# Optimization experiments

Hardware: AMD Instinct MI355X
Metric: run time of the kernel (lower is better)

Reference implementation:

```python
import jax, jax.numpy as jnp
import numpy as np

N_NODES = 50000
N_EDGES = 800000
IN_DIM = 128
HID = 256
BN_EPS = 1e-5
NEG_SLOPE = 0.01


def setup_inputs() -> dict:
    key = jax.random.key(0)
    ks = jax.random.split(key, 8)
    inp = {
        "x": jax.random.normal(ks[0], (N_NODES, IN_DIM), dtype=jnp.float32),
        "src": jax.random.randint(ks[1], (N_EDGES,), 0, N_NODES, dtype=jnp.int32),
        "dst": jax.random.randint(ks[2], (N_EDGES,), 0, N_NODES, dtype=jnp.int32),
        # layer 0 MLP (in->hid->hid) + BN params
        "w1_0": jax.random.normal(ks[3], (IN_DIM, HID), dtype=jnp.float32) / np.sqrt(IN_DIM),
        "b1_0": jnp.zeros((HID,), jnp.float32),
        "w2_0": jax.random.normal(ks[4], (HID, HID), dtype=jnp.float32) / np.sqrt(HID),
        "b2_0": jnp.zeros((HID,), jnp.float32),
        "g0": jnp.ones((HID,), jnp.float32),
        "be0": jnp.zeros((HID,), jnp.float32),
        "m0": jnp.zeros((HID,), jnp.float32),
        "v0": jnp.ones((HID,), jnp.float32),
        # layers 1..2 stacked (hid->hid->hid) + BN params
        "w1_r": jax.random.normal(ks[5], (2, HID, HID), dtype=jnp.float32) / np.sqrt(HID),
        "b1_r": jnp.zeros((2, HID), jnp.float32),
        "w2_r": jax.random.normal(ks[6], (2, HID, HID), dtype=jnp.float32) / np.sqrt(HID),
        "b2_r": jnp.zeros((2, HID), jnp.float32),
        "g_r": jnp.ones((2, HID), jnp.float32),
        "be_r": jnp.zeros((2, HID), jnp.float32),
        "m_r": jnp.zeros((2, HID), jnp.float32),
        "v_r": jnp.ones((2, HID), jnp.float32),
    }
    return inp


def _gin_layer(h, src, dst, w1, b1, w2, b2, g, be, m, v, last):
    # GINConv (eps=0): (1+eps)*h + sum_{j in N(i)} h_j  via gather + scatter-add
    agg = jax.ops.segment_sum(h[src], dst, num_segments=N_NODES)
    z = h + agg
    # 2-layer MLP (dropout is identity in eval)
    z = jax.nn.leaky_relu(z @ w1 + b1, NEG_SLOPE)
    z = z @ w2 + b2
    # BatchNorm1d (eval: running stats)
    z = (z - m) * jax.lax.rsqrt(v + BN_EPS) * g + be
    if not last:
        z = jax.nn.leaky_relu(z, NEG_SLOPE)
    return z


def reference(x, src, dst, w1_0, b1_0, w2_0, b2_0, g0, be0, m0, v0,
              w1_r, b1_r, w2_r, b2_r, g_r, be_r, m_r, v_r):
    h = _gin_layer(x, src, dst, w1_0, b1_0, w2_0, b2_0, g0, be0, m0, v0, last=False)
    for l in range(2):
        h = _gin_layer(h, src, dst, w1_r[l], b1_r[l], w2_r[l], b2_r[l],
                       g_r[l], be_r[l], m_r[l], v_r[l], last=(l == 1))
    return h
```

## Files before the change

kernel.cpp:

```cpp
#include <hip/hip_runtime.h>
#include <hip/hip_bf16.h>
#include <stdint.h>

#define NN 50000
#define NE 800000
#define IND 128
#define HID 256
#define MPAD 50048
#define NBLK 49

#define NCH 64
#define CHSZ 12500
#define NRG 8
#define RGSZ 6250

typedef unsigned int uint32;
typedef unsigned short ushort_t;
typedef __attribute__((ext_vector_type(8))) short short8;
typedef __attribute__((ext_vector_type(4))) float f32x4;

typedef const __attribute__((address_space(1))) void* gptr_t;
typedef __attribute__((address_space(3))) void* lptr_t;

__device__ __forceinline__ ushort_t f2b(float f) {
  uint32 u = __float_as_uint(f);
  u = (u + 0x7fffu + ((u >> 16) & 1u)) >> 16;
  return (ushort_t)u;
}
__device__ __forceinline__ float blo(uint32 u) { return __uint_as_float(u << 16); }
__device__ __forceinline__ float bhi(uint32 u) { return __uint_as_float(u & 0xffff0000u); }
__device__ __forceinline__ uint32 pack2(float a, float b) {
  return (uint32)f2b(a) | ((uint32)f2b(b) << 16);
}

__global__ __launch_bounds__(256) void histp_k(const int* __restrict__ dst,
                                               uint32* __restrict__ partial,
                                               int* __restrict__ rnk) {
  __shared__ uint32 lh[RGSZ];
  const int c = blockIdx.x & (NCH - 1);
  const int rg = blockIdx.x >> 6;
  const int r0 = rg * RGSZ;
  for (int i = threadIdx.x; i < RGSZ; i += 256) lh[i] = 0;
  __syncthreads();
  const int e0 = c * CHSZ;
  for (int i = threadIdx.x; i < CHSZ; i += 256) {
    int e = e0 + i;
    int d = dst[e] - r0;
    if ((unsigned)d < (unsigned)RGSZ) rnk[e] = (int)atomicAdd(&lh[d], 1u);
  }
  __syncthreads();
  uint32* po = partial + (size_t)c * NN + r0;
  for (int i = threadIdx.x; i < RGSZ; i += 256) po[i] = lh[i];
}

__global__ void coff_k(uint32* __restrict__ partial, int* __restrict__ cnt) {
  int bin = blockIdx.x * 256 + threadIdx.x;
  if (bin >= NN) return;
  uint32 run = 0;
#pragma unroll
  for (int c = 0; c < NCH; c++) {
    uint32 t = partial[(size_t)c * NN + bin];
    partial[(size_t)c * NN + bin] = run;
    run += t;
  }
  cnt[bin] = (int)run;
}

__global__ void bsum_k(const int* __restrict__ cnt, int* __restrict__ bsum) {
  __shared__ int ws[16];
  const int tid = threadIdx.x, ln = tid & 63, wv = tid >> 6;
  int i = blockIdx.x * 1024 + tid;
  int v = (i < NN) ? cnt[i] : 0;
#pragma unroll
  for (int d = 32; d; d >>= 1) v += __shfl_down(v, d, 64);
  if (ln == 0) ws[wv] = v;
  __syncthreads();
  if (tid < 16) {
    int s = ws[tid];
#pragma unroll
    for (int d = 8; d; d >>= 1) s += __shfl_down(s, d, 64);
    if (tid == 0) bsum[blockIdx.x] = s;
  }
}

__global__ void bscan_k(int* __restrict__ bsum, int* __restrict__ rp) {
  int tid = threadIdx.x;
  int v = (tid < NBLK) ? bsum[tid] : 0;
  int x = v;
#pragma unroll
  for (int d = 1; d < 64; d <<= 1) {
    int t = __shfl_up(x, d, 64);
    if (tid >= d) x += t;
  }
  if (tid < NBLK) bsum[tid] = x - v;
  if (tid == 0) rp[NN] = NE;
}

__global__ void scan2_k(const int* __restrict__ cnt, const int* __restrict__ bsum,
                        int* __restrict__ rp) {
  __shared__ int ws[16];
  const int tid = threadIdx.x, ln = tid & 63, wv = tid >> 6;
  int i = blockIdx.x * 1024 + tid;
  int v = (i < NN) ? cnt[i] : 0;
  int x = v;
#pragma unroll
  for (int d = 1; d < 64; d <<= 1) {
    int t = __shfl_up(x, d, 64);
    if (ln >= d) x += t;
  }
  if (ln == 63) ws[wv] = x;
  __syncthreads();
  if (tid < 16) {
    int s = ws[tid];
#pragma unroll
    for (int d = 1; d < 16; d <<= 1) {
      int t = __shfl_up(s, d, 64);
      if (tid >= d) s += t;
    }
    ws[tid] = s;
  }
  __syncthreads();
  int excl = x - v + (wv ? ws[wv - 1] : 0) + bsum[blockIdx.x];
  if (i < NN) rp[i] = excl;
}

__global__ void scat2_k(const int* __restrict__ src, const int* __restrict__ dst,
                        const int* __restrict__ rp, const uint32* __restrict__ partial,
                        const int* __restrict__ rnk, int* __restrict__ esrc) {
  int e = blockIdx.x * 256 + threadIdx.x;
  if (e < NE) {
    int d = dst[e];
    int c = e / CHSZ;
    int pos = rp[d] + (int)partial[(size_t)c * NN + d] + rnk[e];
    esrc[pos] = src[e];
  }
}

__global__ void prep_k(const float* __restrict__ w1_0, const float* __restrict__ w2_0,
                       const float* __restrict__ w1_r, const float* __restrict__ w2_r,
                       const float* b1_0, const float* b2_0, const float* g0,
                       const float* be0, const float* m0, const float* v0,
                       const float* b1_r, const float* b2_r, const float* g_r,
                       const float* be_r, const float* m_r, const float* v_r,
                       ushort_t* __restrict__ wt,
                       float* bi1, float* sc2, float* bi2) {
  const int which = blockIdx.y;
  if (which < 6) {
    const int n = blockIdx.x, k = threadIdx.x;
    const float* w; ushort_t* o; int K = HID;
    switch (which) {
      case 0: w = w1_0; o = wt; K = IND; break;
      case 1: w = w2_0; o = wt + HID * IND; break;
      case 2: w = w1_r; o = wt + HID * IND + 1 * HID * HID; break;
      case 3: w = w2_r; o = wt + HID * IND + 2 * HID * HID; break;
      case 4: w = w1_r + HID * HID; o = wt + HID * IND + 3 * HID * HID; break;
      default: w = w2_r + HID * HID; o = wt + HID * IND + 4 * HID * HID; break;
    }
    if (k < K) o[n * K + k] = f2b(w[(size_t)k * HID + n]);
  } else {
    const int l = blockIdx.x;
    if (l >= 3) return;
    const int j = threadIdx.x;
    float b1, b2, g, be, m, v;
    if (l == 0) { b1 = b1_0[j]; b2 = b2_0[j]; g = g0[j]; be = be0[j]; m = m0[j]; v = v0[j]; }
    else { int o = (l - 1) * HID + j; b1 = b1_r[o]; b2 = b2_r[o]; g = g_r[o]; be = be_r[o]; m = m_r[o]; v = v_r[o]; }
    int o = l * HID + j;
    bi1[o] = b1;
    float s = g * rsqrtf(v + 1e-5f);
    sc2[o] = s;
    bi2[o] = (b2 - m) * s + be;
  }
}

__global__ void x2b_k(const float* __restrict__ x, ushort_t* __restrict__ xb) {
  int i = blockIdx.x * 256 + threadIdx.x;
  const int n = NN * IND / 2;
  if (i < n) {
    float2 f = ((const float2*)x)[i];
    ((uint32*)xb)[i] = pack2(f.x, f.y);
  }
}

__global__ void agg256_k(const ushort_t* __restrict__ h, const int* __restrict__ rp,
                         const int* __restrict__ esrc, ushort_t* __restrict__ z) {
  int wid = threadIdx.x >> 6, lane = threadIdx.x & 63;
  int node = blockIdx.x * 4 + wid;
  if (node >= NN) return;
  const uint2* hp = (const uint2*)h;
  uint2 v = hp[(size_t)node * 64 + lane];
  float a0 = blo(v.x), a1 = bhi(v.x), a2 = blo(v.y), a3 = bhi(v.y);
  int e0 = rp[node], e1 = rp[node + 1];
  int e = e0;
  for (; e + 8 <= e1; e += 8) {
    int s[8];
#pragma unroll
    for (int q = 0; q < 8; q++) s[q] = esrc[e + q];
    uint2 u[8];
#pragma unroll
    for (int q = 0; q < 8; q++) u[q] = hp[(size_t)s[q] * 64 + lane];
#pragma unroll
    for (int q = 0; q < 8; q++) {
      a0 += blo(u[q].x); a1 += bhi(u[q].x); a2 += blo(u[q].y); a3 += bhi(u[q].y);
    }
  }
  for (; e < e1; e++) {
    int s = esrc[e];
    uint2 u = hp[(size_t)s * 64 + lane];
    a0 += blo(u.x); a1 += bhi(u.x); a2 += blo(u.y); a3 += bhi(u.y);
  }
  uint2 o; o.x = pack2(a0, a1); o.y = pack2(a2, a3);
  ((uint2*)z)[(size_t)node * 64 + lane] = o;
}

__global__ void agg128_k(const ushort_t* __restrict__ h, const int* __restrict__ rp,
                         const int* __restrict__ esrc, ushort_t* __restrict__ z) {
  int wid = threadIdx.x >> 6, lane = threadIdx.x & 63;
  int node = blockIdx.x * 4 + wid;
  if (node >= NN) return;
  const uint32* hp = (const uint32*)h;
  uint32 v = hp[(size_t)node * 64 + lane];
  float a0 = blo(v), a1 = bhi(v);
  int e0 = rp[node], e1 = rp[node + 1];
  int e = e0;
  for (; e + 8 <= e1; e += 8) {
    int s[8];
#pragma unroll
    for (int q = 0; q < 8; q++) s[q] = esrc[e + q];
    uint32 u[8];
#pragma unroll
    for (int q = 0; q < 8; q++) u[q] = hp[(size_t)s[q] * 64 + lane];
#pragma unroll
    for (int q = 0; q < 8; q++) { a0 += blo(u[q]); a1 += bhi(u[q]); }
  }
  for (; e < e1; e++) {
    int s = esrc[e];
    uint32 u = hp[(size_t)s * 64 + lane];
    a0 += blo(u); a1 += bhi(u);
  }
  ((uint32*)z)[(size_t)node * 64 + lane] = pack2(a0, a1);
}

__global__ __launch_bounds__(256, 2) void fgemm_k(
    const ushort_t* __restrict__ A, const ushort_t* __restrict__ B1t,
    const ushort_t* __restrict__ B2t, const float* __restrict__ bi1,
    const float* __restrict__ sc2, const float* __restrict__ bi2,
    void* __restrict__ out, int K1, int lrelu2, int f32out) {
  __shared__ ushort_t As[64 * 32];
  __shared__ ushort_t Bs[256 * 32];
  __shared__ ushort_t C1s[64 * 264];
  const int tid = threadIdx.x;
  const int lane = tid & 63;
  const int wid = tid >> 6;
  const int m0 = blockIdx.x * 64;
  const int srow = tid >> 2;
  const int sch = (tid & 3) * 8;
  const int fr = lane & 15;
  const int fk = (lane >> 4) * 8;
  const int er = lane >> 4;
  const int ec = lane & 15;

  f32x4 zero = {0.f, 0.f, 0.f, 0.f};
  f32x4 acc[4][4];
#pragma unroll
  for (int i = 0; i < 4; i++)
#pragma unroll
    for (int j = 0; j < 4; j++) acc[i][j] = zero;

  for (int kk = 0; kk < K1; kk += 32) {
    __builtin_amdgcn_global_load_lds((gptr_t)(A + (size_t)(m0 + srow) * K1 + kk + sch),
                                     (lptr_t)(As + srow * 32 + sch), 16, 0, 0);
#pragma unroll
    for (int p = 0; p < 4; p++)
      __builtin_amdgcn_global_load_lds(
          (gptr_t)(B1t + (size_t)(p * 64 + srow) * K1 + kk + sch),
          (lptr_t)(Bs + (p * 64 + srow) * 32 + sch), 16, 0, 0);
    __syncthreads();
    short8 af[4], bfv[4];
#pragma unroll
    for (int i = 0; i < 4; i++)
      af[i] = *(const short8*)(As + (i * 16 + fr) * 32 + fk);
#pragma unroll
    for (int j = 0; j < 4; j++)
      bfv[j] = *(const short8*)(Bs + (wid * 64 + j * 16 + fr) * 32 + fk);
#pragma unroll
    for (int i = 0; i < 4; i++)
#pragma unroll
      for (int j = 0; j < 4; j++)
        acc[i][j] = __builtin_amdgcn_mfma_f32_16x16x32_bf16(af[i], bfv[j], acc[i][j], 0, 0, 0);
    __syncthreads();
  }

#pragma unroll
  for (int j = 0; j < 4; j++) {
    int col = wid * 64 + j * 16 + ec;
    float b = bi1[col];
#pragma unroll
    for (int i = 0; i < 4; i++) {
#pragma unroll
      for (int r = 0; r < 4; r++) {
        int row = i * 16 + er * 4 + r;
        float v = acc[i][j][r] + b;
        v = (v > 0.f) ? v : 0.01f * v;
        C1s[row * 264 + col] = f2b(v);
      }
    }
  }
  __syncthreads();

  f32x4 acc2[4][4];
#pragma unroll
  for (int i = 0; i < 4; i++)
#pragma unroll
    for (int j = 0; j < 4; j++) acc2[i][j] = zero;

  for (int kk = 0; kk < HID; kk += 32) {
#pragma unroll
    for (int p = 0; p < 4; p++)
      __builtin_amdgcn_global_load_lds(
          (gptr_t)(B2t + (size_t)(p * 64 + srow) * HID + kk + sch),
          (lptr_t)(Bs + (p * 64 + srow) * 32 + sch), 16, 0, 0);
    __syncthreads();
    short8 af[4], bfv[4];
#pragma unroll
    for (int i = 0; i < 4; i++)
      af[i] = *(const short8*)(C1s + (i * 16 + fr) * 264 + kk + fk);
#pragma unroll
    for (int j = 0; j < 4; j++)
      bfv[j] = *(const short8*)(Bs + (wid * 64 + j * 16 + fr) * 32 + fk);
#pragma unroll
    for (int i = 0; i < 4; i++)
#pragma unroll
      for (int j = 0; j < 4; j++)
        acc2[i][j] = __builtin_amdgcn_mfma_f32_16x16x32_bf16(af[i], bfv[j], acc2[i][j], 0, 0, 0);
    __syncthreads();
  }

#pragma unroll
  for (int j = 0; j < 4; j++) {
    int col = wid * 64 + j * 16 + ec;
    float s = sc2[col], b = bi2[col];
#pragma unroll
    for (int i = 0; i < 4; i++) {
#pragma unroll
      for (int r = 0; r < 4; r++) {
        int row = m0 + i * 16 + er * 4 + r;
        float v = acc2[i][j][r] * s + b;
        if (lrelu2) v = (v > 0.f) ? v : 0.01f * v;
        if (row < NN) {
          if (f32out) ((float*)out)[(size_t)row * HID + col] = v;
          else        ((ushort_t*)out)[(size_t)row * HID + col] = f2b(v);
        }
      }
    }
  }
}

extern "C" void kernel_launch(void* const* d_in, const int* in_sizes, int n_in,
                              void* d_out, int out_size, void* d_ws, size_t ws_size,
                              hipStream_t stream) {
  const float* x    = (const float*)d_in[0];
  const int*   src  = (const int*)d_in[1];
  const int*   dst  = (const int*)d_in[2];
  const float* w1_0 = (const float*)d_in[3];
  const float* b1_0 = (const float*)d_in[4];
  const float* w2_0 = (const float*)d_in[5];
  const float* b2_0 = (const float*)d_in[6];
  const float* g0   = (const float*)d_in[7];
  const float* be0  = (const float*)d_in[8];
  const float* m0   = (const float*)d_in[9];
  const float* v0   = (const float*)d_in[10];
  const float* w1_r = (const float*)d_in[11];
  const float* b1_r = (const float*)d_in[12];
  const float* w2_r = (const float*)d_in[13];
  const float* b2_r = (const float*)d_in[14];
  const float* g_r  = (const float*)d_in[15];
  const float* be_r = (const float*)d_in[16];
  const float* m_r  = (const float*)d_in[17];
  const float* v_r  = (const float*)d_in[18];

  char* ws = (char*)d_ws;
  size_t off = 0;
  auto alloc = [&](size_t bytes) {
    void* p = ws + off;
    off = (off + bytes + 255) & ~(size_t)255;
    return p;
  };
  ushort_t* bufA  = (ushort_t*)alloc((size_t)MPAD * HID * 2);
  ushort_t* bufB  = (ushort_t*)alloc((size_t)MPAD * HID * 2);
  ushort_t* xb    = (ushort_t*)alloc((size_t)MPAD * IND * 2);
  int*      rp    = (int*)alloc((NN + 1) * sizeof(int));
  int*      cnt   = (int*)alloc(NN * sizeof(int));
  int*      bsum  = (int*)alloc(NBLK * sizeof(int));
  int*      esrc  = (int*)alloc((size_t)NE * sizeof(int));
  ushort_t* wt    = (ushort_t*)alloc(((size_t)HID * IND + 5 * (size_t)HID * HID) * 2);
  float*    bi1   = (float*)alloc(3 * HID * sizeof(float));
  float*    sc2   = (float*)alloc(3 * HID * sizeof(float));
  float*    bi2   = (float*)alloc(3 * HID * sizeof(float));
  (void)ws_size; (void)in_sizes; (void)n_in; (void)out_size;

  uint32* partial = (uint32*)bufA;
  int*    rnk     = (int*)bufB;

  ushort_t* w1_0t = wt;
  ushort_t* w2_0t = wt + HID * IND;
  ushort_t* w1r0t = wt + HID * IND + 1 * HID * HID;
  ushort_t* w2r0t = wt + HID * IND + 2 * HID * HID;
  ushort_t* w1r1t = wt + HID * IND + 3 * HID * HID;
  ushort_t* w2r1t = wt + HID * IND + 4 * HID * HID;

  histp_k<<<NCH * NRG, 256, 0, stream>>>(dst, partial, rnk);
  coff_k<<<(NN + 255) / 256, 256, 0, stream>>>(partial, cnt);
  bsum_k<<<NBLK, 1024, 0, stream>>>(cnt, bsum);
  bscan_k<<<1, 64, 0, stream>>>(bsum, rp);
  scan2_k<<<NBLK, 1024, 0, stream>>>(cnt, bsum, rp);
  scat2_k<<<(NE + 255) / 256, 256, 0, stream>>>(src, dst, rp, partial, rnk, esrc);

  prep_k<<<dim3(HID, 7), 256, 0, stream>>>(w1_0, w2_0, w1_r, w2_r,
                                           b1_0, b2_0, g0, be0, m0, v0,
                                           b1_r, b2_r, g_r, be_r, m_r, v_r,
                                           wt, bi1, sc2, bi2);
  x2b_k<<<(NN * IND / 2 + 255) / 256, 256, 0, stream>>>(x, xb);

  const int GG = MPAD / 64;
  agg128_k<<<NN / 4, 256, 0, stream>>>(xb, rp, esrc, bufA);
  fgemm_k<<<GG, 256, 0, stream>>>(bufA, w1_0t, w2_0t, bi1, sc2, bi2, bufB, IND, 1, 0);
  agg256_k<<<NN / 4, 256, 0, stream>>>(bufB, rp, esrc, bufA);
  fgemm_k<<<GG, 256, 0, stream>>>(bufA, w1r0t, w2r0t, bi1 + HID, sc2 + HID, bi2 + HID, bufB, HID, 1, 0);
  agg256_k<<<NN / 4, 256, 0, stream>>>(bufB, rp, esrc, bufA);
  fgemm_k<<<GG, 256, 0, stream>>>(bufA, w1r1t, w2r1t, bi1 + 2 * HID, sc2 + 2 * HID, bi2 + 2 * HID, d_out, HID, 0, 1);
}
```

Measured before the change: 465.0 us.

## Double-buffer LDS tiles in fused MLP GEMM and template on K

The fused two-layer GEMM kernel now keeps two LDS buffers for the A and B tiles. The next k-tile's global-to-LDS load is issued before the MFMAs on the current tile, and the first second-stage weight tile is prefetched before the intermediate epilogue. This hides global load latency behind compute and removes one barrier per k-step. The input K dimension becomes a template parameter so loop bounds are compile-time constants. The cost is more LDS per block (about 74KB versus about 54KB), which could limit occupancy, and correctness depends on the barrier also waiting for the async LDS loads.

```diff
diff --git a/kernel.cpp b/kernel.cpp
--- a/kernel.cpp
+++ b/kernel.cpp
@@ -240,13 +240,14 @@
   ((uint32*)z)[(size_t)node * 64 + lane] = pack2(a0, a1);
 }
 
+template<int K1>
 __global__ __launch_bounds__(256, 2) void fgemm_k(
     const ushort_t* __restrict__ A, const ushort_t* __restrict__ B1t,
     const ushort_t* __restrict__ B2t, const float* __restrict__ bi1,
     const float* __restrict__ sc2, const float* __restrict__ bi2,
-    void* __restrict__ out, int K1, int lrelu2, int f32out) {
-  __shared__ ushort_t As[64 * 32];
-  __shared__ ushort_t Bs[256 * 32];
+    void* __restrict__ out, int lrelu2, int f32out) {
+  __shared__ ushort_t As[2][64 * 32];
+  __shared__ ushort_t Bs[2][256 * 32];
   __shared__ ushort_t C1s[64 * 264];
   const int tid = threadIdx.x;
   const int lane = tid & 63;
@@ -258,30 +259,45 @@
   const int fk = (lane >> 4) * 8;
   const int er = lane >> 4;
   const int ec = lane & 15;
-
-  f32x4 zero = {0.f, 0.f, 0.f, 0.f};
-  f32x4 acc[4][4];
-#pragma unroll
-  for (int i = 0; i < 4; i++)
-#pragma unroll
-    for (int j = 0; j < 4; j++) acc[i][j] = zero;
-
-  for (int kk = 0; kk < K1; kk += 32) {
+  constexpr int T1 = K1 / 32;
+
+  auto stage1 = [&](int b, int kk) {
     __builtin_amdgcn_global_load_lds((gptr_t)(A + (size_t)(m0 + srow) * K1 + kk + sch),
-                                     (lptr_t)(As + srow * 32 + sch), 16, 0, 0);
+                                     (lptr_t)(&As[b][srow * 32 + sch]), 16, 0, 0);
 #pragma unroll
     for (int p = 0; p < 4; p++)
       __builtin_amdgcn_global_load_lds(
           (gptr_t)(B1t + (size_t)(p * 64 + srow) * K1 + kk + sch),
-          (lptr_t)(Bs + (p * 64 + srow) * 32 + sch), 16, 0, 0);
-    __syncthreads();
+          (lptr_t)(&Bs[b][(p * 64 + srow) * 32 + sch]), 16, 0, 0);
+  };
+  auto stage2 = [&](int b, int kk) {
+#pragma unroll
+    for (int p = 0; p < 4; p++)
+      __builtin_amdgcn_global_load_lds(
+          (gptr_t)(B2t + (size_t)(p * 64 + srow) * HID + kk + sch),
+          (lptr_t)(&Bs[b][(p * 64 + srow) * 32 + sch]), 16, 0, 0);
+  };
+
+  f32x4 zero = {0.f, 0.f, 0.f, 0.f};
+  f32x4 acc[4][4];
+#pragma unroll
+  for (int i = 0; i < 4; i++)
+#pragma unroll
+    for (int j = 0; j < 4; j++) acc[i][j] = zero;
+
+  stage1(0, 0);
+  __syncthreads();
+#pragma unroll 2
+  for (int t = 0; t < T1; t++) {
+    const int b = t & 1;
+    if (t + 1 < T1) stage1(b ^ 1, (t + 1) * 32);
     short8 af[4], bfv[4];
 #pragma unroll
     for (int i = 0; i < 4; i++)
-      af[i] = *(const short8*)(As + (i * 16 + fr) * 32 + fk);
+      af[i] = *(const short8*)(&As[b][(i * 16 + fr) * 32 + fk]);
 #pragma unroll
     for (int j = 0; j < 4; j++)
-      bfv[j] = *(const short8*)(Bs + (wid * 64 + j * 16 + fr) * 32 + fk);
+      bfv[j] = *(const short8*)(&Bs[b][(wid * 64 + j * 16 + fr) * 32 + fk]);
 #pragma unroll
     for (int i = 0; i < 4; i++)
 #pragma unroll
@@ -289,6 +305,8 @@
         acc[i][j] = __builtin_amdgcn_mfma_f32_16x16x32_bf16(af[i], bfv[j], acc[i][j], 0, 0, 0);
     __syncthreads();
   }
+
+  stage2(0, 0);
 
 #pragma unroll
   for (int j = 0; j < 4; j++) {
@@ -313,20 +331,18 @@
 #pragma unroll
     for (int j = 0; j < 4; j++) acc2[i][j] = zero;
 
-  for (int kk = 0; kk < HID; kk += 32) {
-#pragma unroll
-    for (int p = 0; p < 4; p++)
-      __builtin_amdgcn_global_load_lds(
-          (gptr_t)(B2t + (size_t)(p * 64 + srow) * HID + kk + sch),
-          (lptr_t)(Bs + (p * 64 + srow) * 32 + sch), 16, 0, 0);
-    __syncthreads();
+#pragma unroll 2
+  for (int t = 0; t < 8; t++) {
+    const int b = t & 1;
+    if (t + 1 < 8) stage2(b ^ 1, (t + 1) * 32);
+    const int kk = t * 32;
     short8 af[4], bfv[4];
 #pragma unroll
     for (int i = 0; i < 4; i++)
       af[i] = *(const short8*)(C1s + (i * 16 + fr) * 264 + kk + fk);
 #pragma unroll
     for (int j = 0; j < 4; j++)
-      bfv[j] = *(const short8*)(Bs + (wid * 64 + j * 16 + fr) * 32 + fk);
+      bfv[j] = *(const short8*)(&Bs[b][(wid * 64 + j * 16 + fr) * 32 + fk]);
 #pragma unroll
     for (int i = 0; i < 4; i++)
 #pragma unroll
@@ -423,9 +439,9 @@
 
   const int GG = MPAD / 64;
   agg128_k<<<NN / 4, 256, 0, stream>>>(xb, rp, esrc, bufA);
-  fgemm_k<<<GG, 256, 0, stream>>>(bufA, w1_0t, w2_0t, bi1, sc2, bi2, bufB, IND, 1, 0);
+  fgemm_k<IND><<<GG, 256, 0, stream>>>(bufA, w1_0t, w2_0t, bi1, sc2, bi2, bufB, 1, 0);
   agg256_k<<<NN / 4, 256, 0, stream>>>(bufB, rp, esrc, bufA);
-  fgemm_k<<<GG, 256, 0, stream>>>(bufA, w1r0t, w2r0t, bi1 + HID, sc2 + HID, bi2 + HID, bufB, HID, 1, 0);
+  fgemm_k<HID><<<GG, 256, 0, stream>>>(bufA, w1r0t, w2r0t, bi1 + HID, sc2 + HID, bi2 + HID, bufB, 1, 0);
   agg256_k<<<NN / 4, 256, 0, stream>>>(bufB, rp, esrc, bufA);
-  fgemm_k<<<GG, 256, 0, stream>>>(bufA, w1r1t, w2r1t, bi1 + 2 * HID, sc2 + 2 * HID, bi2 + 2 * HID, d_out, HID, 0, 1);
-}
+  fgemm_k<HID><<<GG, 256, 0, stream>>>(bufA, w1r1t, w2r1t, bi1 + 2 * HID, sc2 + 2 * HID, bi2 + 2 * HID, d_out, 0, 1);
+}
```

Result: no change. 458.6 us (-1.4%).
